# Optimization experiments

Measured on AMD Instinct MI355X. Metric: run time of the kernel, lower is better.

Reference implementation:

```python
import jax, jax.numpy as jnp
import numpy as np

N_EMBD = 1024
N_HEAD = 16
HEAD_SIZE = N_EMBD // N_HEAD  # 64


def setup_inputs() -> dict:
    key = jax.random.key(0)
    k1, k2, k3, k4 = jax.random.split(key, 4)
    B, T = 4, 4096
    x = jax.random.normal(k1, (B, T, N_EMBD), dtype=jnp.float32)
    scale = 1.0 / np.sqrt(N_EMBD)
    # Linear(n_embd, head_size, bias=False): store as [C, H] so projection is x @ W
    Wk = jax.random.normal(k2, (N_EMBD, HEAD_SIZE), dtype=jnp.float32) * scale
    Wq = jax.random.normal(k3, (N_EMBD, HEAD_SIZE), dtype=jnp.float32) * scale
    Wv = jax.random.normal(k4, (N_EMBD, HEAD_SIZE), dtype=jnp.float32) * scale
    decay_factor = jnp.array([-0.5], dtype=jnp.float32)
    return {"x": x, "Wk": Wk, "Wq": Wq, "Wv": Wv, "decay_factor": decay_factor}


def reference(x, Wk, Wq, Wv, decay_factor):
    B, T, C = x.shape
    H = Wk.shape[1]
    k = x @ Wk  # [B,T,H]
    q = x @ Wq  # [B,T,H]
    v = x @ Wv  # [B,T,H]
    wei = jnp.einsum('bth,bsh->bts', q, k) * (H ** -0.5)  # [B,T,T]
    idx = jnp.arange(T)
    dist = jnp.minimum(idx[None, :] - idx[:, None], 0)  # j - i, clamped max=0
    ripple_bias = dist.astype(x.dtype) * jnp.abs(decay_factor[0])
    wei = wei + ripple_bias[None, :, :]
    causal = idx[None, :] <= idx[:, None]  # tril mask [T,T]
    wei = jnp.where(causal[None, :, :], wei, -jnp.inf)
    wei = jax.nn.softmax(wei, axis=-1)
    return jnp.einsum('bts,bsh->bth', wei, v)
```

## Files before the change

### kernel.cpp

```cpp
#include <hip/hip_runtime.h>

typedef short bf16x8 __attribute__((ext_vector_type(8)));
typedef float f32x4 __attribute__((ext_vector_type(4)));

#define TT 4096
#define CC 1024
#define HH 64
#define MTOT 16384

static __device__ __forceinline__ unsigned short f2bf(float f) {
  unsigned int u = __float_as_uint(f);
  unsigned int r = (u + 0x7FFFu + ((u >> 16) & 1u)) >> 16;
  return (unsigned short)r;
}

static __device__ __forceinline__ unsigned int pack_bf2(float lo, float hi) {
  unsigned int ul = __float_as_uint(lo) + 0x8000u;
  unsigned int uh = __float_as_uint(hi) + 0x8000u;
  return __builtin_amdgcn_perm(uh, ul, 0x07060302u);
}

typedef const __attribute__((address_space(1))) void gvoid;
typedef __attribute__((address_space(3))) void svoid;
static __device__ __forceinline__ void gll16(const void* g, void* l) {
  __builtin_amdgcn_global_load_lds((gvoid*)g, (svoid*)l, 16, 0, 0);
}

#define WAITVM(N) asm volatile("s_waitcnt vmcnt(" #N ")" ::: "memory")

__global__ void prep_wt(const float* __restrict__ Wk, const float* __restrict__ Wq,
                        const float* __restrict__ Wv, unsigned short* __restrict__ Wt) {
  __shared__ float T[64][65];
  const int mat = blockIdx.x >> 4;
  const int kt = blockIdx.x & 15;
  const float* src = (mat == 0) ? Wk : ((mat == 1) ? Wq : Wv);
#pragma unroll
  for (int i = 0; i < 4; ++i) {
    int c = i * 256 + threadIdx.x;
    int row = c >> 4, col = (c & 15) * 4;
    f32x4 v = *(const f32x4*)&src[(size_t)(kt * 64 + row) * HH + col];
    T[col + 0][row] = v[0];
    T[col + 1][row] = v[1];
    T[col + 2][row] = v[2];
    T[col + 3][row] = v[3];
  }
  __syncthreads();
#pragma unroll
  for (int i = 0; i < 2; ++i) {
    int c2 = i * 256 + threadIdx.x;
    int row = c2 >> 3, k0 = (c2 & 7) * 8;
    union { bf16x8 v; unsigned short h[8]; } pk;
#pragma unroll
    for (int j = 0; j < 8; ++j) pk.h[j] = f2bf(T[row][k0 + j]);
    *(bf16x8*)&Wt[(size_t)(mat * 64 + row) * CC + kt * 64 + k0] = pk.v;
  }
}

__global__ __launch_bounds__(512, 2) void proj_kernel(
    const float* __restrict__ x, const unsigned short* __restrict__ Wt,
    unsigned short* __restrict__ kb, unsigned short* __restrict__ qb,
    unsigned short* __restrict__ vt) {
  extern __shared__ __align__(16) char smem[];
  float* Xl = (float*)smem;
  unsigned short* Bl = (unsigned short*)(smem + 49152);

  const int tid = threadIdx.x;
  const int lane = tid & 63;
  const int w = tid >> 6;
  const int r = lane & 15, g = lane >> 4;
  const int rowgrp = w >> 1;
  const int colbase = (w & 1) * 96;
  const int m0 = blockIdx.x * 64;

  const float* xsrcs[2];
#pragma unroll
  for (int j = 0; j < 2; ++j) {
    int c = j * 512 + tid;
    int row = c >> 4, s = c & 15;
    xsrcs[j] = x + (size_t)(m0 + row) * CC + (((s & 8) | ((s & 7) ^ (row & 7))) * 4);
  }
  const unsigned short* bsrcs[3];
#pragma unroll
  for (int j = 0; j < 3; ++j) {
    int cb = j * 512 + tid;
    int row = cb >> 3, s = cb & 7;
    bsrcs[j] = Wt + (size_t)row * CC + ((s ^ (row & 7)) * 8);
  }

  f32x4 acc[6];
#pragma unroll
  for (int n = 0; n < 6; ++n) { f32x4 z = {0.f, 0.f, 0.f, 0.f}; acc[n] = z; }

  auto stage = [&](int t, int buf) {
    float* xb = Xl + buf * 4096;
    unsigned short* bb = Bl + buf * 12288;
#pragma unroll
    for (int j = 0; j < 2; ++j)
      gll16(xsrcs[j] + t * 64, xb + (j * 512 + w * 64) * 4);
#pragma unroll
    for (int j = 0; j < 3; ++j)
      gll16(bsrcs[j] + t * 64, bb + (size_t)(j * 512 + w * 64) * 8);
  };

  const int rr = rowgrp * 16 + r;
  const int rb = rr * 64;
  const int rx = rr & 7;

  auto body = [&](int buf) {
    const float* xb = Xl + buf * 4096;
    const unsigned short* bb = Bl + buf * 12288;
    bf16x8 bfr[2][6];
#pragma unroll
    for (int ks = 0; ks < 2; ++ks)
#pragma unroll
      for (int n = 0; n < 6; ++n) {
        int col = colbase + 16 * n + r;
        bfr[ks][n] = *(const bf16x8*)&bb[col * 64 + (((ks * 4 + g) ^ (col & 7)) * 8)];
      }
#pragma unroll
    for (int ks = 0; ks < 2; ++ks) {
      int s0 = ks * 8 + 2 * g;
      f32x4 v0 = *(const f32x4*)&xb[rb + (((s0 & 8) | ((s0 & 7) ^ rx)) * 4)];
      f32x4 v1 = *(const f32x4*)&xb[rb + ((((s0 + 1) & 8) | (((s0 + 1) & 7) ^ rx)) * 4)];
      union { bf16x8 v; unsigned int u[4]; } af;
      af.u[0] = pack_bf2(v0.x, v0.y);
      af.u[1] = pack_bf2(v0.z, v0.w);
      af.u[2] = pack_bf2(v1.x, v1.y);
      af.u[3] = pack_bf2(v1.z, v1.w);
#pragma unroll
      for (int n = 0; n < 6; ++n)
        acc[n] = __builtin_amdgcn_mfma_f32_16x16x32_bf16(af.v, bfr[ks][n], acc[n], 0, 0, 0);
    }
  };

  stage(0, 0);
  stage(1, 1);

  for (int t = 0; t < 15; ++t) {
    WAITVM(5);
    __builtin_amdgcn_s_barrier();
    if (t + 2 < 16) stage(t + 2, (t + 2) % 3);
    body(t % 3);
  }
  WAITVM(0);
  __builtin_amdgcn_s_barrier();
  body(0);

  float* Vt = (float*)(smem + 73728);
#pragma unroll
  for (int n = 0; n < 6; ++n) {
#pragma unroll
    for (int i = 0; i < 4; ++i) {
      int row = rowgrp * 16 + 4 * g + i;
      int col = colbase + 16 * n + r;
      float val = acc[n][i];
      if (col < 64) {
        kb[(size_t)(m0 + row) * HH + col] = f2bf(val);
      } else if (col < 128) {
        qb[(size_t)(m0 + row) * HH + (col - 64)] = f2bf(val);
      } else {
        Vt[(col - 128) * 65 + row] = val;
      }
    }
  }
  __syncthreads();
  {
    int dim = tid >> 3, t8 = (tid & 7) * 8;
    union { bf16x8 v; unsigned short h[8]; } pk;
#pragma unroll
    for (int j = 0; j < 8; ++j) pk.h[j] = f2bf(Vt[dim * 65 + t8 + j]);
    int b = m0 >> 12;
    int tt = (m0 & (TT - 1)) + t8;
    *(bf16x8*)&vt[(((size_t)b * HH + dim) << 12) + tt] = pk.v;
  }
}

__global__ __launch_bounds__(256, 2) void attn_kernel(
    const unsigned short* __restrict__ qb, const unsigned short* __restrict__ kb,
    const unsigned short* __restrict__ vt, const float* __restrict__ decayp,
    float* __restrict__ out) {
  extern __shared__ __align__(16) char smem[];
  unsigned short* Kl = (unsigned short*)smem;
  unsigned short* Vl = Kl + 16384;
  unsigned short* Pl = Vl + 16384;
  float* Ol = (float*)(smem + 65536);
  float* Ml = (float*)(smem + 65536 + 8704);
  float* Ll = Ml + 32;

  const int tid = threadIdx.x;
  const int lane = tid & 63;
  const int w = tid >> 6;
  const int r = lane & 15, g = lane >> 4;
  const int qh = w & 1;
  const int kvg = w >> 1;

  const int batch = blockIdx.x & 3;
  const int qt = blockIdx.x >> 2;
  const int qbase = qt * 32;
  const int qw = qbase + qh * 16;
  const int qrow = qw + r;

  const float decay = fabsf(decayp[0]);

  const unsigned short* qbb = qb + (size_t)batch * TT * HH;
  const unsigned short* kbb = kb + (size_t)batch * TT * HH;
  const unsigned short* vbb = vt + (size_t)batch * HH * TT;

  const unsigned short* qp = qbb + (size_t)qrow * HH;
  bf16x8 aq0 = *(const bf16x8*)(qp + 8 * g);
  bf16x8 aq1 = *(const bf16x8*)(qp + 32 + 8 * g);

  int t0 = 0;
  if (decay > 1e-8f) {
    float wf = 25.f / decay;
    if (wf < (float)TT) {
      int W = (int)wf + 1;
      int lo = qbase - W;
      if (lo < 0) lo = 0;
      t0 = lo >> 6;
    }
  }
  const int t1 = (qbase + 31) >> 6;
  const int nsteps = (t1 - t0 + 2) >> 1;

  const unsigned short* ksrc[4];
  const unsigned short* vsrc[4];
#pragma unroll
  for (int j = 0; j < 4; ++j) {
    int c = j * 256 + tid;
    int th = c >> 9;
    int cc = c & 511;
    int row = cc >> 3, sl = cc & 7;
    ksrc[j] = kbb + (size_t)((t0 + th) * 64 + row) * HH + ((sl ^ (row & 7)) * 8);
    vsrc[j] = vbb + (size_t)row * TT + (t0 + th) * 64 + ((sl ^ (row & 7)) * 8);
  }

  auto stage = [&](int s, int buf) {
#pragma unroll
    for (int j = 0; j < 4; ++j) {
      gll16(ksrc[j] + (size_t)s * 8192, Kl + buf * 8192 + (j * 256 + w * 64) * 8);
      gll16(vsrc[j] + s * 128, Vl + buf * 8192 + (j * 256 + w * 64) * 8);
    }
  };

  float m = -1e30f, lsum = 0.f;
  f32x4 o[4];
#pragma unroll
  for (int n = 0; n < 4; ++n) { f32x4 z = {0.f, 0.f, 0.f, 0.f}; o[n] = z; }

  stage(0, 0);

  for (int s = 0; s < nsteps; ++s) {
    if (s + 1 < nsteps) { stage(s + 1, (s + 1) & 1); WAITVM(8); }
    else { WAITVM(0); }
    __builtin_amdgcn_s_barrier();

    const int myt = t0 + 2 * s + kvg;
    if (myt <= t1) {
      const unsigned short* Kb = Kl + (s & 1) * 8192 + kvg * 4096;
      const unsigned short* Vb = Vl + (s & 1) * 8192 + kvg * 4096;
      const int kv0 = myt * 64;

      f32x4 sacc[4];
      __builtin_amdgcn_s_setprio(1);
#pragma unroll
      for (int t = 0; t < 4; ++t) {
        f32x4 z = {0.f, 0.f, 0.f, 0.f};
        int kvr = 16 * t + r;
        bf16x8 b0 = *(const bf16x8*)&Kb[kvr * 64 + ((g ^ (kvr & 7)) * 8)];
        bf16x8 b1 = *(const bf16x8*)&Kb[kvr * 64 + (((4 + g) ^ (kvr & 7)) * 8)];
        z = __builtin_amdgcn_mfma_f32_16x16x32_bf16(b0, aq0, z, 0, 0, 0);
        sacc[t] = __builtin_amdgcn_mfma_f32_16x16x32_bf16(b1, aq1, z, 0, 0, 0);
      }
      __builtin_amdgcn_s_setprio(0);

      float p[4][4];
      float rmax = -1e30f;
#pragma unroll
      for (int t = 0; t < 4; ++t)
#pragma unroll
        for (int i = 0; i < 4; ++i) {
          int kv = kv0 + 16 * t + 4 * g + i;
          float sv = sacc[t][i] * 0.125f + decay * (float)(kv - qrow);
          if (kv > qrow) sv = -1e30f;
          p[t][i] = sv;
          rmax = fmaxf(rmax, sv);
        }
      rmax = fmaxf(rmax, __shfl_xor(rmax, 16));
      rmax = fmaxf(rmax, __shfl_xor(rmax, 32));
      float mn = fmaxf(m, rmax);
      float al = __expf(m - mn);
      m = mn;
      float rs = 0.f;
#pragma unroll
      for (int t = 0; t < 4; ++t)
#pragma unroll
        for (int i = 0; i < 4; ++i) {
          float e = __expf(p[t][i] - mn);
          p[t][i] = e;
          rs += e;
        }
      rs += __shfl_xor(rs, 16);
      rs += __shfl_xor(rs, 32);
      lsum = lsum * al + rs;
#pragma unroll
      for (int n = 0; n < 4; ++n) {
        o[n][0] *= al; o[n][1] *= al; o[n][2] *= al; o[n][3] *= al;
      }

      char* P = (char*)(Pl + w * 1024) + r * 128;
#pragma unroll
      for (int t = 0; t < 4; ++t) {
        uint2 u;
        u.x = pack_bf2(p[t][0], p[t][1]);
        u.y = pack_bf2(p[t][2], p[t][3]);
        *(uint2*)(P + ((t ^ (r & 3)) * 32) + g * 8) = u;
      }
      bf16x8 pb0 = *(const bf16x8*)(P + (((g >> 1) ^ (r & 3)) * 32) + (g & 1) * 16);
      bf16x8 pb1 = *(const bf16x8*)(P + ((((g >> 1) + 2) ^ (r & 3)) * 32) + (g & 1) * 16);

      __builtin_amdgcn_s_setprio(1);
#pragma unroll
      for (int n = 0; n < 4; ++n) {
        int dim = 16 * n + r;
        bf16x8 v0 = *(const bf16x8*)&Vb[dim * 64 + ((g ^ (dim & 7)) * 8)];
        bf16x8 v1 = *(const bf16x8*)&Vb[dim * 64 + (((4 + g) ^ (dim & 7)) * 8)];
        o[n] = __builtin_amdgcn_mfma_f32_16x16x32_bf16(v0, pb0, o[n], 0, 0, 0);
        o[n] = __builtin_amdgcn_mfma_f32_16x16x32_bf16(v1, pb1, o[n], 0, 0, 0);
      }
      __builtin_amdgcn_s_setprio(0);
    }
    __builtin_amdgcn_s_barrier();
  }

  const int orow = qh * 16 + r;
  if (kvg == 1) {
    if (lane < 16) { Ml[orow] = m; Ll[orow] = lsum; }
#pragma unroll
    for (int n = 0; n < 4; ++n)
#pragma unroll
      for (int i = 0; i < 4; ++i)
        Ol[orow * 68 + 16 * n + 4 * g + i] = o[n][i];
  }
  __syncthreads();
  if (kvg == 0) {
    float m2 = Ml[orow], l2 = Ll[orow];
    float M = fmaxf(m, m2);
    float e1 = __expf(m - M), e2 = __expf(m2 - M);
    float inv = 1.f / (lsum * e1 + l2 * e2);
#pragma unroll
    for (int n = 0; n < 4; ++n)
#pragma unroll
      for (int i = 0; i < 4; ++i) {
        int d = 16 * n + 4 * g + i;
        Ol[orow * 68 + d] = (o[n][i] * e1 + Ol[orow * 68 + d] * e2) * inv;
      }
  }
  __syncthreads();

  float* ob = out + (size_t)batch * TT * HH;
#pragma unroll
  for (int j = 0; j < 2; ++j) {
    int c = j * 256 + tid;
    int row = c >> 4, q4 = (c & 15) * 4;
    f32x4 vv = *(const f32x4*)&Ol[row * 68 + q4];
    *(f32x4*)&ob[(size_t)(qbase + row) * HH + q4] = vv;
  }
}

extern "C" void kernel_launch(void* const* d_in, const int* in_sizes, int n_in,
                              void* d_out, int out_size, void* d_ws, size_t ws_size,
                              hipStream_t stream) {
  const float* x = (const float*)d_in[0];
  const float* Wk = (const float*)d_in[1];
  const float* Wq = (const float*)d_in[2];
  const float* Wv = (const float*)d_in[3];
  const float* decay = (const float*)d_in[4];
  float* out = (float*)d_out;

  unsigned short* kb = (unsigned short*)d_ws;
  unsigned short* qbw = kb + (size_t)MTOT * HH;
  unsigned short* vt = qbw + (size_t)MTOT * HH;
  unsigned short* Wt = vt + (size_t)MTOT * HH;

  prep_wt<<<dim3(48), dim3(256), 0, stream>>>(Wk, Wq, Wv, Wt);
  proj_kernel<<<dim3(256), dim3(512), 120 * 1024, stream>>>(x, Wt, kb, qbw, vt);
  attn_kernel<<<dim3(512), dim3(256), 74496, stream>>>(qbw, kb, vt, decay, out);
}
```

Measured before the change: 30.92 us.

## Load projection A operand directly into registers instead of staging via LDS

The projection kernel no longer stages x tiles through shared memory with async global-to-LDS copies. Each thread now loads its own x fragment straight into registers in a three-deep register ring, while only the weight tiles still go through LDS. This shrinks shared memory, removes the LDS round trip for x, and raises the occupancy hint. The cost is more registers per thread and x loads that are less coalesced, since each lane reads 16-byte chunks along its own row.

```diff
diff --git a/kernel.cpp b/kernel.cpp
--- a/kernel.cpp
+++ b/kernel.cpp
@@ -56,13 +56,12 @@
   }
 }
 
-__global__ __launch_bounds__(512, 2) void proj_kernel(
+__global__ __launch_bounds__(512, 4) void proj_kernel(
     const float* __restrict__ x, const unsigned short* __restrict__ Wt,
     unsigned short* __restrict__ kb, unsigned short* __restrict__ qb,
     unsigned short* __restrict__ vt) {
   extern __shared__ __align__(16) char smem[];
-  float* Xl = (float*)smem;
-  unsigned short* Bl = (unsigned short*)(smem + 49152);
+  unsigned short* Bl = (unsigned short*)smem;
 
   const int tid = threadIdx.x;
   const int lane = tid & 63;
@@ -72,13 +71,6 @@
   const int colbase = (w & 1) * 96;
   const int m0 = blockIdx.x * 64;
 
-  const float* xsrcs[2];
-#pragma unroll
-  for (int j = 0; j < 2; ++j) {
-    int c = j * 512 + tid;
-    int row = c >> 4, s = c & 15;
-    xsrcs[j] = x + (size_t)(m0 + row) * CC + (((s & 8) | ((s & 7) ^ (row & 7))) * 4);
-  }
   const unsigned short* bsrcs[3];
 #pragma unroll
   for (int j = 0; j < 3; ++j) {
@@ -87,66 +79,69 @@
     bsrcs[j] = Wt + (size_t)row * CC + ((s ^ (row & 7)) * 8);
   }
 
+  const int rr = rowgrp * 16 + r;
+  const float* aptr = x + (size_t)(m0 + rr) * CC + 8 * g;
+
   f32x4 acc[6];
 #pragma unroll
   for (int n = 0; n < 6; ++n) { f32x4 z = {0.f, 0.f, 0.f, 0.f}; acc[n] = z; }
 
-  auto stage = [&](int t, int buf) {
-    float* xb = Xl + buf * 4096;
+  f32x4 av[3][4];
+
+  auto stageB = [&](int t, int buf) {
     unsigned short* bb = Bl + buf * 12288;
-#pragma unroll
-    for (int j = 0; j < 2; ++j)
-      gll16(xsrcs[j] + t * 64, xb + (j * 512 + w * 64) * 4);
 #pragma unroll
     for (int j = 0; j < 3; ++j)
       gll16(bsrcs[j] + t * 64, bb + (size_t)(j * 512 + w * 64) * 8);
   };
 
-  const int rr = rowgrp * 16 + r;
-  const int rb = rr * 64;
-  const int rx = rr & 7;
-
-  auto body = [&](int buf) {
-    const float* xb = Xl + buf * 4096;
-    const unsigned short* bb = Bl + buf * 12288;
-    bf16x8 bfr[2][6];
-#pragma unroll
-    for (int ks = 0; ks < 2; ++ks)
-#pragma unroll
-      for (int n = 0; n < 6; ++n) {
-        int col = colbase + 16 * n + r;
-        bfr[ks][n] = *(const bf16x8*)&bb[col * 64 + (((ks * 4 + g) ^ (col & 7)) * 8)];
-      }
-#pragma unroll
-    for (int ks = 0; ks < 2; ++ks) {
-      int s0 = ks * 8 + 2 * g;
-      f32x4 v0 = *(const f32x4*)&xb[rb + (((s0 & 8) | ((s0 & 7) ^ rx)) * 4)];
-      f32x4 v1 = *(const f32x4*)&xb[rb + ((((s0 + 1) & 8) | (((s0 + 1) & 7) ^ rx)) * 4)];
-      union { bf16x8 v; unsigned int u[4]; } af;
-      af.u[0] = pack_bf2(v0.x, v0.y);
-      af.u[1] = pack_bf2(v0.z, v0.w);
-      af.u[2] = pack_bf2(v1.x, v1.y);
-      af.u[3] = pack_bf2(v1.z, v1.w);
-#pragma unroll
-      for (int n = 0; n < 6; ++n)
-        acc[n] = __builtin_amdgcn_mfma_f32_16x16x32_bf16(af.v, bfr[ks][n], acc[n], 0, 0, 0);
-    }
-  };
-
-  stage(0, 0);
-  stage(1, 1);
-
-  for (int t = 0; t < 15; ++t) {
-    WAITVM(5);
+#pragma unroll
+  for (int j = 0; j < 4; ++j)
+    av[0][j] = *(const f32x4*)(aptr + ((j >> 1) * 32 + (j & 1) * 4));
+  stageB(0, 0);
+#pragma unroll
+  for (int j = 0; j < 4; ++j)
+    av[1][j] = *(const f32x4*)(aptr + 64 + ((j >> 1) * 32 + (j & 1) * 4));
+  stageB(1, 1);
+
+#pragma unroll
+  for (int t = 0; t < 16; ++t) {
+    if (t < 15) { WAITVM(7); }
+    else { WAITVM(0); }
     __builtin_amdgcn_s_barrier();
-    if (t + 2 < 16) stage(t + 2, (t + 2) % 3);
-    body(t % 3);
-  }
-  WAITVM(0);
-  __builtin_amdgcn_s_barrier();
-  body(0);
-
-  float* Vt = (float*)(smem + 73728);
+    if (t + 2 < 16) {
+#pragma unroll
+      for (int j = 0; j < 4; ++j)
+        av[(t + 2) % 3][j] = *(const f32x4*)(aptr + (t + 2) * 64 + ((j >> 1) * 32 + (j & 1) * 4));
+      stageB(t + 2, (t + 2) % 3);
+    }
+    {
+      const unsigned short* bb = Bl + (t % 3) * 12288;
+      bf16x8 bfr[2][6];
+#pragma unroll
+      for (int ks = 0; ks < 2; ++ks)
+#pragma unroll
+        for (int n = 0; n < 6; ++n) {
+          int col = colbase + 16 * n + r;
+          bfr[ks][n] = *(const bf16x8*)&bb[col * 64 + (((ks * 4 + g) ^ (col & 7)) * 8)];
+        }
+#pragma unroll
+      for (int ks = 0; ks < 2; ++ks) {
+        f32x4 v0 = av[t % 3][2 * ks];
+        f32x4 v1 = av[t % 3][2 * ks + 1];
+        union { bf16x8 v; unsigned int u[4]; } af;
+        af.u[0] = pack_bf2(v0.x, v0.y);
+        af.u[1] = pack_bf2(v0.z, v0.w);
+        af.u[2] = pack_bf2(v1.x, v1.y);
+        af.u[3] = pack_bf2(v1.z, v1.w);
+#pragma unroll
+        for (int n = 0; n < 6; ++n)
+          acc[n] = __builtin_amdgcn_mfma_f32_16x16x32_bf16(af.v, bfr[ks][n], acc[n], 0, 0, 0);
+      }
+    }
+  }
+
+  float* Vt = (float*)(smem + 24576);
 #pragma unroll
   for (int n = 0; n < 6; ++n) {
 #pragma unroll
@@ -384,6 +379,6 @@
   unsigned short* Wt = vt + (size_t)MTOT * HH;
 
   prep_wt<<<dim3(48), dim3(256), 0, stream>>>(Wk, Wq, Wv, Wt);
-  proj_kernel<<<dim3(256), dim3(512), 120 * 1024, stream>>>(x, Wt, kb, qbw, vt);
+  proj_kernel<<<dim3(256), dim3(512), 73728, stream>>>(x, Wt, kb, qbw, vt);
   attn_kernel<<<dim3(512), dim3(256), 74496, stream>>>(qbw, kb, vt, decay, out);
 }
```

Result: slower. 40.69 us (+31.6%).

## Enlarge attention query tile to 64 rows with 512 threads, drop double buffering

Applied to the files above, without the earlier changes.

Each attention block now covers 64 query rows using 8 waves (4 query groups by 2 KV groups) instead of 32 rows with 4 waves. The grid halves to 256 blocks and the block-to-batch mapping changes. Each K/V tile loaded into shared memory is reused across twice as many queries, which cuts global K/V traffic. The K/V double buffer is replaced by a single synchronous buffer, so load latency is no longer overlapped with compute, and 256 blocks may underfill the GPU.

```diff
diff --git a/kernel.cpp b/kernel.cpp
--- a/kernel.cpp
+++ b/kernel.cpp
@@ -175,29 +175,28 @@
   }
 }
 
-__global__ __launch_bounds__(256, 2) void attn_kernel(
+__global__ __launch_bounds__(512, 4) void attn_kernel(
     const unsigned short* __restrict__ qb, const unsigned short* __restrict__ kb,
     const unsigned short* __restrict__ vt, const float* __restrict__ decayp,
     float* __restrict__ out) {
   extern __shared__ __align__(16) char smem[];
   unsigned short* Kl = (unsigned short*)smem;
-  unsigned short* Vl = Kl + 16384;
-  unsigned short* Pl = Vl + 16384;
-  float* Ol = (float*)(smem + 65536);
-  float* Ml = (float*)(smem + 65536 + 8704);
-  float* Ll = Ml + 32;
+  unsigned short* Vl = (unsigned short*)(smem + 16384);
+  unsigned short* Pl = (unsigned short*)(smem + 32768);
+  float* Ol = (float*)(smem + 49152);
+  float* Ml = (float*)(smem + 66560);
+  float* Ll = (float*)(smem + 66816);
 
   const int tid = threadIdx.x;
   const int lane = tid & 63;
   const int w = tid >> 6;
   const int r = lane & 15, g = lane >> 4;
-  const int qh = w & 1;
-  const int kvg = w >> 1;
-
-  const int batch = blockIdx.x & 3;
-  const int qt = blockIdx.x >> 2;
-  const int qbase = qt * 32;
-  const int qw = qbase + qh * 16;
+  const int qh = w & 3;
+  const int kvg = w >> 2;
+  const int batch = blockIdx.x >> 6;
+  const int mt = blockIdx.x & 63;
+  const int qbase0 = mt * 64;
+  const int qw = qbase0 + qh * 16;
   const int qrow = qw + r;
 
   const float decay = fabsf(decayp[0]);
@@ -215,19 +214,19 @@
     float wf = 25.f / decay;
     if (wf < (float)TT) {
       int W = (int)wf + 1;
-      int lo = qbase - W;
+      int lo = qbase0 - W;
       if (lo < 0) lo = 0;
       t0 = lo >> 6;
     }
   }
-  const int t1 = (qbase + 31) >> 6;
+  const int t1 = mt;
   const int nsteps = (t1 - t0 + 2) >> 1;
 
-  const unsigned short* ksrc[4];
-  const unsigned short* vsrc[4];
-#pragma unroll
-  for (int j = 0; j < 4; ++j) {
-    int c = j * 256 + tid;
+  const unsigned short* ksrc[2];
+  const unsigned short* vsrc[2];
+#pragma unroll
+  for (int j = 0; j < 2; ++j) {
+    int c = j * 512 + tid;
     int th = c >> 9;
     int cc = c & 511;
     int row = cc >> 3, sl = cc & 7;
@@ -235,11 +234,11 @@
     vsrc[j] = vbb + (size_t)row * TT + (t0 + th) * 64 + ((sl ^ (row & 7)) * 8);
   }
 
-  auto stage = [&](int s, int buf) {
-#pragma unroll
-    for (int j = 0; j < 4; ++j) {
-      gll16(ksrc[j] + (size_t)s * 8192, Kl + buf * 8192 + (j * 256 + w * 64) * 8);
-      gll16(vsrc[j] + s * 128, Vl + buf * 8192 + (j * 256 + w * 64) * 8);
+  auto stage = [&](int s) {
+#pragma unroll
+    for (int j = 0; j < 2; ++j) {
+      gll16(ksrc[j] + (size_t)s * 8192, Kl + (j * 512 + w * 64) * 8);
+      gll16(vsrc[j] + s * 128, Vl + (j * 512 + w * 64) * 8);
     }
   };
 
@@ -248,17 +247,15 @@
 #pragma unroll
   for (int n = 0; n < 4; ++n) { f32x4 z = {0.f, 0.f, 0.f, 0.f}; o[n] = z; }
 
-  stage(0, 0);
-
   for (int s = 0; s < nsteps; ++s) {
-    if (s + 1 < nsteps) { stage(s + 1, (s + 1) & 1); WAITVM(8); }
-    else { WAITVM(0); }
-    __builtin_amdgcn_s_barrier();
+    stage(s);
+    WAITVM(0);
+    __syncthreads();
 
     const int myt = t0 + 2 * s + kvg;
     if (myt <= t1) {
-      const unsigned short* Kb = Kl + (s & 1) * 8192 + kvg * 4096;
-      const unsigned short* Vb = Vl + (s & 1) * 8192 + kvg * 4096;
+      const unsigned short* Kb = Kl + kvg * 4096;
+      const unsigned short* Vb = Vl + kvg * 4096;
       const int kv0 = myt * 64;
 
       f32x4 sacc[4];
@@ -311,10 +308,10 @@
       char* P = (char*)(Pl + w * 1024) + r * 128;
 #pragma unroll
       for (int t = 0; t < 4; ++t) {
-        uint2 u;
-        u.x = pack_bf2(p[t][0], p[t][1]);
-        u.y = pack_bf2(p[t][2], p[t][3]);
-        *(uint2*)(P + ((t ^ (r & 3)) * 32) + g * 8) = u;
+        uint2 uu;
+        uu.x = pack_bf2(p[t][0], p[t][1]);
+        uu.y = pack_bf2(p[t][2], p[t][3]);
+        *(uint2*)(P + ((t ^ (r & 3)) * 32) + g * 8) = uu;
       }
       bf16x8 pb0 = *(const bf16x8*)(P + (((g >> 1) ^ (r & 3)) * 32) + (g & 1) * 16);
       bf16x8 pb1 = *(const bf16x8*)(P + ((((g >> 1) + 2) ^ (r & 3)) * 32) + (g & 1) * 16);
@@ -330,7 +327,7 @@
       }
       __builtin_amdgcn_s_setprio(0);
     }
-    __builtin_amdgcn_s_barrier();
+    __syncthreads();
   }
 
   const int orow = qh * 16 + r;
@@ -358,13 +355,13 @@
   }
   __syncthreads();
 
-  float* ob = out + (size_t)batch * TT * HH;
+  float* ob = out + (size_t)batch * TT * HH + (size_t)qbase0 * HH;
 #pragma unroll
   for (int j = 0; j < 2; ++j) {
-    int c = j * 256 + tid;
+    int c = j * 512 + tid;
     int row = c >> 4, q4 = (c & 15) * 4;
     f32x4 vv = *(const f32x4*)&Ol[row * 68 + q4];
-    *(f32x4*)&ob[(size_t)(qbase + row) * HH + q4] = vv;
+    *(f32x4*)&ob[(size_t)row * HH + q4] = vv;
   }
 }
 
@@ -385,5 +382,5 @@
 
   prep_wt<<<dim3(48), dim3(256), 0, stream>>>(Wk, Wq, Wv, Wt);
   proj_kernel<<<dim3(256), dim3(512), 120 * 1024, stream>>>(x, Wt, kb, qbw, vt);
-  attn_kernel<<<dim3(512), dim3(256), 74496, stream>>>(qbw, kb, vt, decay, out);
-}
+  attn_kernel<<<dim3(256), dim3(512), 67072, stream>>>(qbw, kb, vt, decay, out);
+}
```

New measurement: 30.58 us, median of 2. About the same (-1.1%).
